# Kernel tuning notes

Hardware: AMD Instinct MI355X
Metric: run time of the kernel (lower is better)

The kernel has to match this reference:

```python
import jax, jax.numpy as jnp
import numpy as np

B, S, D, H = 4, 2048, 1024, 16
DK = D // H

def setup_inputs() -> dict:
    key = jax.random.key(0)
    ks = jax.random.split(key, 8)
    scale = 1.0 / np.sqrt(D)
    return {
        "q": jax.random.normal(ks[0], (B, S, D), jnp.float32),
        "k": jax.random.normal(ks[1], (B, S, D), jnp.float32),
        "v": jax.random.normal(ks[2], (B, S, D), jnp.float32),
        "wq": jax.random.normal(ks[3], (D, D), jnp.float32) * scale,
        "bq": jnp.zeros((D,), jnp.float32),
        "wk": jax.random.normal(ks[4], (D, D), jnp.float32) * scale,
        "bk": jnp.zeros((D,), jnp.float32),
        "wv": jax.random.normal(ks[5], (D, D), jnp.float32) * scale,
        "bv": jnp.zeros((D,), jnp.float32),
        "wo": jax.random.normal(ks[6], (D, D), jnp.float32) * scale,
        "bo": jnp.zeros((D,), jnp.float32),
    }

def reference(q, k, v, wq, bq, wk, bk, wv, bv, wo, bo):
    b, s, _ = q.shape
    # projections; split heads -> [b, h, s, d_k]
    def proj(x, w, bias):
        y = x @ w + bias
        return y.reshape(b, -1, H, DK).transpose(0, 2, 1, 3)
    qh, kh, vh = proj(q, wq, bq), proj(k, wk, bk), proj(v, wv, bv)
    scores = jnp.einsum("bhqd,bhkd->bhqk", qh, kh) / np.sqrt(DK).astype(jnp.float32)
    attn = jax.nn.softmax(scores, axis=-1)  # dropout = identity (eval mode)
    out = jnp.einsum("bhqk,bhkd->bhqd", attn, vh)
    out = out.transpose(0, 2, 1, 3).reshape(b, s, D)
    return out @ wo + bo
```

## Files before the change

kernel.cpp:

```cpp
#include <hip/hip_runtime.h>
#include <hip/hip_bf16.h>

#define B_   4
#define S_   2048
#define D_   1024
#define H_   16
#define DK_  64
#define NTOK 8192

typedef __bf16 bf16_t;
typedef __bf16 bf16x8 __attribute__((ext_vector_type(8)));
typedef __bf16 bf16x4 __attribute__((ext_vector_type(4)));
typedef short  s16x4  __attribute__((ext_vector_type(4)));
typedef float  f32x4  __attribute__((ext_vector_type(4)));

__device__ __forceinline__ void gll16(const void* g, void* l) {
  __builtin_amdgcn_global_load_lds(
      (const __attribute__((address_space(1))) void*)g,
      (__attribute__((address_space(3))) void*)l,
      16, 0, 0);
}

__device__ __forceinline__ f32x4 mfma32(bf16x8 a, bf16x8 b, f32x4 c) {
  return __builtin_amdgcn_mfma_f32_16x16x32_bf16(a, b, c, 0, 0, 0);
}

__device__ __forceinline__ f32x4 mfma16k(bf16x4 a, bf16x4 b, f32x4 c) {
#if defined(__HIP_DEVICE_COMPILE__)
  return __builtin_amdgcn_mfma_f32_16x16x16bf16_1k(
      __builtin_bit_cast(s16x4, a), __builtin_bit_cast(s16x4, b), c, 0, 0, 0);
#else
  (void)a; (void)b;
  return c;
#endif
}

__device__ __forceinline__ float fast_exp2(float x) {
#if defined(__HIP_DEVICE_COMPILE__) && __has_builtin(__builtin_amdgcn_exp2f)
  return __builtin_amdgcn_exp2f(x);
#else
  return exp2f(x);
#endif
}

__global__ __launch_bounds__(256) void tobf16(
    const float* __restrict__ q, const float* __restrict__ k,
    const float* __restrict__ v, bf16_t* __restrict__ o) {
  const float* src = (blockIdx.z == 0) ? q : (blockIdx.z == 1) ? k : v;
  bf16_t* dst = o + (size_t)blockIdx.z * 8388608;
  size_t i = ((size_t)blockIdx.x * 256 + threadIdx.x) * 4;
  float4 x = *(const float4*)&src[i];
  bf16x4 y;
  y[0] = (bf16_t)x.x; y[1] = (bf16_t)x.y;
  y[2] = (bf16_t)x.z; y[3] = (bf16_t)x.w;
  *(bf16x4*)&dst[i] = y;
}

__global__ __launch_bounds__(256) void prep_weights(
    const float* __restrict__ wq, const float* __restrict__ wk,
    const float* __restrict__ wv, const float* __restrict__ wo,
    bf16_t* __restrict__ wtHi) {
  const int z = blockIdx.z;
  const float* W = (z == 0) ? wq : (z == 1) ? wk : (z == 2) ? wv : wo;
  const int k0 = blockIdx.x * 64;
  const int n0 = blockIdx.y * 64;
  const int t = threadIdx.x;
  __shared__ float T[64][65];
#pragma unroll
  for (int rr = 0; rr < 4; ++rr) {
    int row = rr * 16 + (t >> 4);
    int cc = (t & 15) * 4;
    const float4 v = *(const float4*)&W[(size_t)(k0 + row) * D_ + n0 + cc];
    T[row][cc + 0] = v.x; T[row][cc + 1] = v.y;
    T[row][cc + 2] = v.z; T[row][cc + 3] = v.w;
  }
  __syncthreads();
  const int n = t >> 2;
  const int kc = (t & 3) * 16;
  bf16x8 h0, h1;
#pragma unroll
  for (int j = 0; j < 16; ++j) {
    float vv = T[kc + j][n];
    if (j < 8) h0[j] = (bf16_t)vv;
    else       h1[j - 8] = (bf16_t)vv;
  }
  size_t ofs = (size_t)z * 1048576 + (size_t)(n0 + n) * D_ + k0 + kc;
  *(bf16x8*)&wtHi[ofs] = h0; *(bf16x8*)&wtHi[ofs + 8] = h1;
}

__global__ __launch_bounds__(256) void gemm_qkv_bf16(
    const bf16_t* __restrict__ Abf,
    const float* __restrict__ bq, const float* __restrict__ bk,
    const float* __restrict__ bv,
    const bf16_t* __restrict__ wtHi, bf16_t* __restrict__ outQKV) {
  const int z = blockIdx.z;
  const bf16_t* A   = Abf + (size_t)z * 8388608;
  const float* bias = (z == 0) ? bq : (z == 1) ? bk : bv;
  const bf16_t* WHi = wtHi + (size_t)z * 1048576;
  bf16_t* Out = outQKV + (size_t)z * 8388608;

  const int row0 = blockIdx.x * 128;
  const int col0 = blockIdx.y * 128;
  const int t = threadIdx.x;
  const int w = t >> 6, L = t & 63;
  const int m = L & 15, g = L >> 4;

  __shared__ __align__(16) bf16_t As2[128 * 32];
  __shared__ __align__(16) bf16_t Whi_s[128 * 32];

  f32x4 acc[4][4];
#pragma unroll
  for (int i = 0; i < 4; ++i)
#pragma unroll
    for (int j = 0; j < 4; ++j) acc[i][j] = (f32x4){0.f, 0.f, 0.f, 0.f};

  const int aw0 = (w & 1) * 64;
  const int bw0 = (w >> 1) * 64;

  for (int kt = 0; kt < 32; ++kt) {
    const int k0 = kt * 32;
#pragma unroll
    for (int rr = 0; rr < 2; ++rr) {
      int lin16 = rr * 256 + t;
      int n = lin16 >> 2;
      int c = (lin16 & 3) ^ ((n >> 1) & 3);
      gll16(&A[(size_t)(row0 + n) * D_ + k0 + c * 8], &As2[rr * 2048 + w * 512]);
      gll16(&WHi[(size_t)(col0 + n) * D_ + k0 + c * 8], &Whi_s[rr * 2048 + w * 512]);
    }
    __syncthreads();

    bf16x8 af[4], wh[4];
#pragma unroll
    for (int it = 0; it < 4; ++it) {
      int row = aw0 + it * 16 + m;
      int sl = (g ^ ((m >> 1) & 3)) * 8;
      af[it] = *(const bf16x8*)&As2[row * 32 + sl];
    }
#pragma unroll
    for (int jt = 0; jt < 4; ++jt) {
      int n = bw0 + jt * 16 + m;
      int sl = (g ^ ((m >> 1) & 3)) * 8;
      wh[jt] = *(const bf16x8*)&Whi_s[n * 32 + sl];
    }
#pragma unroll
    for (int it = 0; it < 4; ++it)
#pragma unroll
      for (int jt = 0; jt < 4; ++jt)
        acc[it][jt] = mfma32(af[it], wh[jt], acc[it][jt]);
    __syncthreads();
  }
#pragma unroll
  for (int jt = 0; jt < 4; ++jt) {
    int col = col0 + bw0 + jt * 16 + m;
    float bcol = bias[col];
    int h = col >> 6, d = col & 63;
#pragma unroll
    for (int it = 0; it < 4; ++it) {
      if (z != 2) {
#pragma unroll
        for (int r = 0; r < 4; ++r) {
          int row = row0 + aw0 + it * 16 + g * 4 + r;
          int b = row >> 11, s = row & 2047;
          Out[((size_t)((b * H_ + h) * S_ + s)) * DK_ + d] =
              (bf16_t)(acc[it][jt][r] + bcol);
        }
      } else {
        int row = row0 + aw0 + it * 16 + g * 4;
        int b = row >> 11, s = row & 2047;
        bf16x4 p4;
#pragma unroll
        for (int r = 0; r < 4; ++r) p4[r] = (bf16_t)(acc[it][jt][r] + bcol);
        *(bf16x4*)&Out[((size_t)((b * H_ + h) * DK_ + d)) * S_ + s] = p4;
      }
    }
  }
}

__global__ __launch_bounds__(256) void gemm_qkv_f32(
    const float* __restrict__ Aq, const float* __restrict__ Ak,
    const float* __restrict__ Av,
    const float* __restrict__ bq, const float* __restrict__ bk,
    const float* __restrict__ bv,
    const bf16_t* __restrict__ wtHi, bf16_t* __restrict__ outQKV) {
  const int z = blockIdx.z;
  const float* A    = (z == 0) ? Aq : (z == 1) ? Ak : Av;
  const float* bias = (z == 0) ? bq : (z == 1) ? bk : bv;
  const bf16_t* WHi = wtHi + (size_t)z * 1048576;
  bf16_t* Out = outQKV + (size_t)z * 8388608;

  const int row0 = blockIdx.x * 128;
  const int col0 = blockIdx.y * 128;
  const int t = threadIdx.x;
  const int w = t >> 6, L = t & 63;
  const int m = L & 15, g = L >> 4;

  __shared__ __align__(16) float  As[128 * 32];
  __shared__ __align__(16) bf16_t Whi_s[128 * 32];

  f32x4 acc[4][4];
#pragma unroll
  for (int i = 0; i < 4; ++i)
#pragma unroll
    for (int j = 0; j < 4; ++j) acc[i][j] = (f32x4){0.f, 0.f, 0.f, 0.f};

  const int aw0 = (w & 1) * 64;
  const int bw0 = (w >> 1) * 64;

  for (int kt = 0; kt < 32; ++kt) {
    const int k0 = kt * 32;
#pragma unroll
    for (int rr = 0; rr < 4; ++rr) {
      int lin16 = rr * 256 + t;
      int row = lin16 >> 3;
      int c = (lin16 & 7) ^ (row & 7);
      gll16(&A[(size_t)(row0 + row) * D_ + k0 + c * 4], &As[rr * 1024 + w * 256]);
    }
#pragma unroll
    for (int rr = 0; rr < 2; ++rr) {
      int lin16 = rr * 256 + t;
      int n = lin16 >> 2;
      int c = (lin16 & 3) ^ ((n >> 1) & 3);
      gll16(&WHi[(size_t)(col0 + n) * D_ + k0 + c * 8], &Whi_s[rr * 2048 + w * 512]);
    }
    __syncthreads();

    bf16x8 af[4], wh[4];
#pragma unroll
    for (int it = 0; it < 4; ++it) {
      int row = aw0 + it * 16 + m;
      const f32x4* p = (const f32x4*)&As[row * 32];
      f32x4 x0 = p[(2 * g) ^ (m & 7)];
      f32x4 x1 = p[(2 * g + 1) ^ (m & 7)];
      bf16x8 a;
      a[0] = (bf16_t)x0.x; a[1] = (bf16_t)x0.y; a[2] = (bf16_t)x0.z; a[3] = (bf16_t)x0.w;
      a[4] = (bf16_t)x1.x; a[5] = (bf16_t)x1.y; a[6] = (bf16_t)x1.z; a[7] = (bf16_t)x1.w;
      af[it] = a;
    }
#pragma unroll
    for (int jt = 0; jt < 4; ++jt) {
      int n = bw0 + jt * 16 + m;
      int sl = (g ^ ((m >> 1) & 3)) * 8;
      wh[jt] = *(const bf16x8*)&Whi_s[n * 32 + sl];
    }
#pragma unroll
    for (int it = 0; it < 4; ++it)
#pragma unroll
      for (int jt = 0; jt < 4; ++jt)
        acc[it][jt] = mfma32(af[it], wh[jt], acc[it][jt]);
    __syncthreads();
  }
#pragma unroll
  for (int jt = 0; jt < 4; ++jt) {
    int col = col0 + bw0 + jt * 16 + m;
    float bcol = bias[col];
    int h = col >> 6, d = col & 63;
#pragma unroll
    for (int it = 0; it < 4; ++it) {
      if (z != 2) {
#pragma unroll
        for (int r = 0; r < 4; ++r) {
          int row = row0 + aw0 + it * 16 + g * 4 + r;
          int b = row >> 11, s = row & 2047;
          Out[((size_t)((b * H_ + h) * S_ + s)) * DK_ + d] =
              (bf16_t)(acc[it][jt][r] + bcol);
        }
      } else {
        int row = row0 + aw0 + it * 16 + g * 4;
        int b = row >> 11, s = row & 2047;
        bf16x4 p4;
#pragma unroll
        for (int r = 0; r < 4; ++r) p4[r] = (bf16_t)(acc[it][jt][r] + bcol);
        *(bf16x4*)&Out[((size_t)((b * H_ + h) * DK_ + d)) * S_ + s] = p4;
      }
    }
  }
}

__global__ __launch_bounds__(256) void attn(
    const bf16_t* __restrict__ Qh, const bf16_t* __restrict__ Kh,
    const bf16_t* __restrict__ VhT, bf16_t* __restrict__ Ohi) {
  const int bh = blockIdx.y;
  const int q0 = blockIdx.x * 128;
  const int t = threadIdx.x, w = t >> 6, L = t & 63;
  const int m = L & 15, g = L >> 4;

  __shared__ __align__(16) bf16_t Ks[64 * 64];
  __shared__ __align__(16) bf16_t Vt[64 * 64];

  const size_t qbase = (size_t)bh * S_ * DK_;
  const size_t vbase = (size_t)bh * DK_ * S_;

  bf16x8 qf[2][2];
#pragma unroll
  for (int qt = 0; qt < 2; ++qt)
#pragma unroll
    for (int kc = 0; kc < 2; ++kc) {
      int srow = q0 + w * 32 + qt * 16 + m;
      bf16x8 v = *(const bf16x8*)&Qh[qbase + (size_t)srow * DK_ + kc * 32 + g * 8];
#pragma unroll
      for (int j = 0; j < 8; ++j) v[j] = (bf16_t)(0.18033688f * (float)v[j]);
      qf[qt][kc] = v;
    }

  const bf16x4 ones = {(bf16_t)1.f, (bf16_t)1.f, (bf16_t)1.f, (bf16_t)1.f};

  f32x4 oacc[2][4];
  f32x4 lacc[2];
#pragma unroll
  for (int qt = 0; qt < 2; ++qt) {
#pragma unroll
    for (int dt = 0; dt < 4; ++dt) oacc[qt][dt] = (f32x4){0.f, 0.f, 0.f, 0.f};
    lacc[qt] = (f32x4){0.f, 0.f, 0.f, 0.f};
  }

  for (int kv0 = 0; kv0 < S_; kv0 += 64) {
#pragma unroll
    for (int rr = 0; rr < 2; ++rr) {
      int lin16 = rr * 256 + t;
      int rrow = lin16 >> 3;
      int c = (lin16 & 7) ^ (rrow & 7);
      gll16(&Kh[qbase + (size_t)(kv0 + rrow) * DK_ + c * 8], &Ks[rr * 2048 + w * 512]);
      gll16(&VhT[vbase + (size_t)rrow * S_ + kv0 + c * 8], &Vt[rr * 2048 + w * 512]);
    }
    __syncthreads();

    f32x4 sc[2][4];
#pragma unroll
    for (int kvt = 0; kvt < 4; ++kvt) {
      int n = kvt * 16 + m;
      bf16x8 kf0 = *(const bf16x8*)&Ks[n * 64 + ((g) ^ (n & 7)) * 8];
      bf16x8 kf1 = *(const bf16x8*)&Ks[n * 64 + ((4 + g) ^ (n & 7)) * 8];
#pragma unroll
      for (int qt = 0; qt < 2; ++qt) {
        f32x4 z4 = (f32x4){0.f, 0.f, 0.f, 0.f};
        z4 = mfma32(kf0, qf[qt][0], z4);
        z4 = mfma32(kf1, qf[qt][1], z4);
        sc[qt][kvt] = z4;
      }
    }

    bf16x4 pb[2][4];
#pragma unroll
    for (int qt = 0; qt < 2; ++qt)
#pragma unroll
      for (int kvt = 0; kvt < 4; ++kvt) {
        bf16x4 p4;
#pragma unroll
        for (int r = 0; r < 4; ++r) p4[r] = (bf16_t)fast_exp2(sc[qt][kvt][r]);
        pb[qt][kvt] = p4;
      }

#pragma unroll
    for (int kvt = 0; kvt < 4; ++kvt) {
#pragma unroll
      for (int qt = 0; qt < 2; ++qt)
        lacc[qt] = mfma16k(ones, pb[qt][kvt], lacc[qt]);
#pragma unroll
      for (int dt = 0; dt < 4; ++dt) {
        int d = dt * 16 + m;
        int sl = (kvt * 2 + (g >> 1)) ^ (d & 7);
        bf16x4 vf = *(const bf16x4*)&Vt[d * 64 + sl * 8 + (g & 1) * 4];
#pragma unroll
        for (int qt = 0; qt < 2; ++qt)
          oacc[qt][dt] = mfma16k(vf, pb[qt][kvt], oacc[qt][dt]);
      }
    }
    __syncthreads();
  }

  const int b = bh >> 4, h = bh & 15;
#pragma unroll
  for (int qt = 0; qt < 2; ++qt) {
    float inv = 1.f / lacc[qt][0];
    int srow = q0 + w * 32 + qt * 16 + m;
    size_t rowofs = ((size_t)(b * S_ + srow)) * D_ + h * DK_;
#pragma unroll
    for (int dt = 0; dt < 4; ++dt) {
      bf16x4 hp;
#pragma unroll
      for (int r = 0; r < 4; ++r) hp[r] = (bf16_t)(oacc[qt][dt][r] * inv);
      *(bf16x4*)&Ohi[rowofs + dt * 16 + g * 4] = hp;
    }
  }
}

__global__ __launch_bounds__(256) void gemm_out(
    const bf16_t* __restrict__ Ahi, const bf16_t* __restrict__ wtHi,
    const float* __restrict__ bias, float* __restrict__ Out) {
  const bf16_t* WHi = wtHi + (size_t)3 * 1048576;
  const int row0 = blockIdx.x * 128;
  const int col0 = blockIdx.y * 128;
  const int t = threadIdx.x;
  const int w = t >> 6, L = t & 63;
  const int m = L & 15, g = L >> 4;

  __shared__ __align__(16) bf16_t Ahi_s[128 * 32];
  __shared__ __align__(16) bf16_t Whi_s[128 * 32];

  f32x4 acc[4][4];
#pragma unroll
  for (int i = 0; i < 4; ++i)
#pragma unroll
    for (int j = 0; j < 4; ++j) acc[i][j] = (f32x4){0.f, 0.f, 0.f, 0.f};

  const int aw0 = (w & 1) * 64;
  const int bw0 = (w >> 1) * 64;

  for (int kt = 0; kt < 32; ++kt) {
    const int k0 = kt * 32;
#pragma unroll
    for (int rr = 0; rr < 2; ++rr) {
      int lin16 = rr * 256 + t;
      int n = lin16 >> 2;
      int c = (lin16 & 3) ^ ((n >> 1) & 3);
      gll16(&Ahi[(size_t)(row0 + n) * D_ + k0 + c * 8], &Ahi_s[rr * 2048 + w * 512]);
      gll16(&WHi[(size_t)(col0 + n) * D_ + k0 + c * 8], &Whi_s[rr * 2048 + w * 512]);
    }
    __syncthreads();

    bf16x8 ah[4], wh[4];
#pragma unroll
    for (int it = 0; it < 4; ++it) {
      int row = aw0 + it * 16 + m;
      int sl = (g ^ ((m >> 1) & 3)) * 8;
      ah[it] = *(const bf16x8*)&Ahi_s[row * 32 + sl];
    }
#pragma unroll
    for (int jt = 0; jt < 4; ++jt) {
      int n = bw0 + jt * 16 + m;
      int sl = (g ^ ((m >> 1) & 3)) * 8;
      wh[jt] = *(const bf16x8*)&Whi_s[n * 32 + sl];
    }
#pragma unroll
    for (int it = 0; it < 4; ++it)
#pragma unroll
      for (int jt = 0; jt < 4; ++jt)
        acc[it][jt] = mfma32(ah[it], wh[jt], acc[it][jt]);
    __syncthreads();
  }
#pragma unroll
  for (int jt = 0; jt < 4; ++jt) {
    int col = col0 + bw0 + jt * 16 + m;
    float bcol = bias[col];
#pragma unroll
    for (int it = 0; it < 4; ++it)
#pragma unroll
      for (int r = 0; r < 4; ++r) {
        int row = row0 + aw0 + it * 16 + g * 4 + r;
        Out[(size_t)row * D_ + col] = acc[it][jt][r] + bcol;
      }
  }
}

extern "C" void kernel_launch(void* const* d_in, const int* in_sizes, int n_in,
                              void* d_out, int out_size, void* d_ws, size_t ws_size,
                              hipStream_t stream) {
  const float* q  = (const float*)d_in[0];
  const float* k  = (const float*)d_in[1];
  const float* v  = (const float*)d_in[2];
  const float* wq = (const float*)d_in[3];
  const float* bq = (const float*)d_in[4];
  const float* wk = (const float*)d_in[5];
  const float* bk = (const float*)d_in[6];
  const float* wv = (const float*)d_in[7];
  const float* bv = (const float*)d_in[8];
  const float* wo = (const float*)d_in[9];
  const float* bo = (const float*)d_in[10];
  float* out = (float*)d_out;

  char* ws = (char*)d_ws;
  bf16_t* wtHi = (bf16_t*)(ws);
  bf16_t* QKVh = (bf16_t*)(ws + (8ull << 20));
  bf16_t* Ohi  = (bf16_t*)(ws + (56ull << 20));
  bf16_t* Abf  = (bf16_t*)(ws + (56ull << 20));

  const bool big = ws_size >= (104ull << 20);

  hipLaunchKernelGGL(prep_weights, dim3(16, 16, 4), dim3(256), 0, stream,
                     wq, wk, wv, wo, wtHi);
  if (big) {
    hipLaunchKernelGGL(tobf16, dim3(8192, 1, 3), dim3(256), 0, stream,
                       q, k, v, Abf);
    hipLaunchKernelGGL(gemm_qkv_bf16, dim3(64, 8, 3), dim3(256), 0, stream,
                       Abf, bq, bk, bv, wtHi, QKVh);
  } else {
    hipLaunchKernelGGL(gemm_qkv_f32, dim3(64, 8, 3), dim3(256), 0, stream,
                       q, k, v, bq, bk, bv, wtHi, QKVh);
  }
  hipLaunchKernelGGL(attn, dim3(16, 64), dim3(256), 0, stream,
                     QKVh, QKVh + 8388608, QKVh + 16777216, Ohi);
  hipLaunchKernelGGL(gemm_out, dim3(64, 8), dim3(256), 0, stream,
                     Ohi, wtHi, bo, out);
}
```

Baseline: 373.3 us.

## Switch attention kernel to 32x32x16 MFMA with permlane32 swap for P operand

Rewrites the attention inner loop to use 32x32x16 bf16 MFMA tiles instead of 16x16x32 for QK^T and 16x16x16 for PV. Scores are exponentiated, packed to bf16 and rearranged across lane halves with permlane32_swap so the score accumulator layout can be fed straight back as the B operand of the PV and row-sum MFMAs. Launch bounds now request two blocks per CU. The aim is fewer MFMA issues and fewer LDS reads per tile, at the cost of larger 16-wide accumulators and higher register pressure.

```diff
diff --git a/kernel.cpp b/kernel.cpp
--- a/kernel.cpp
+++ b/kernel.cpp
@@ -11,8 +11,11 @@
 typedef __bf16 bf16_t;
 typedef __bf16 bf16x8 __attribute__((ext_vector_type(8)));
 typedef __bf16 bf16x4 __attribute__((ext_vector_type(4)));
-typedef short  s16x4  __attribute__((ext_vector_type(4)));
+typedef __bf16 bf16x2 __attribute__((ext_vector_type(2)));
 typedef float  f32x4  __attribute__((ext_vector_type(4)));
+typedef float  f32x16 __attribute__((ext_vector_type(16)));
+typedef unsigned u32x4 __attribute__((ext_vector_type(4)));
+typedef int    i32x2  __attribute__((ext_vector_type(2)));
 
 __device__ __forceinline__ void gll16(const void* g, void* l) {
   __builtin_amdgcn_global_load_lds(
@@ -25,10 +28,9 @@
   return __builtin_amdgcn_mfma_f32_16x16x32_bf16(a, b, c, 0, 0, 0);
 }
 
-__device__ __forceinline__ f32x4 mfma16k(bf16x4 a, bf16x4 b, f32x4 c) {
+__device__ __forceinline__ f32x16 mfma32x32(bf16x8 a, bf16x8 b, f32x16 c) {
 #if defined(__HIP_DEVICE_COMPILE__)
-  return __builtin_amdgcn_mfma_f32_16x16x16bf16_1k(
-      __builtin_bit_cast(s16x4, a), __builtin_bit_cast(s16x4, b), c, 0, 0, 0);
+  return __builtin_amdgcn_mfma_f32_32x32x16_bf16(a, b, c, 0, 0, 0);
 #else
   (void)a; (void)b;
   return c;
@@ -41,6 +43,47 @@
 #else
   return exp2f(x);
 #endif
+}
+
+__device__ __forceinline__ f32x16 zero16() {
+  f32x16 z;
+#pragma unroll
+  for (int i = 0; i < 16; ++i) z[i] = 0.f;
+  return z;
+}
+
+__device__ __forceinline__ unsigned pkbf(float lo, float hi) {
+  bf16x2 t;
+  t[0] = (bf16_t)lo;
+  t[1] = (bf16_t)hi;
+  return __builtin_bit_cast(unsigned, t);
+}
+
+__device__ __forceinline__ void plswap(unsigned &x, unsigned &y) {
+#if defined(__HIP_DEVICE_COMPILE__)
+  i32x2 r = __builtin_amdgcn_permlane32_swap((int)x, (int)y, false, false);
+  x = (unsigned)r[0];
+  y = (unsigned)r[1];
+#endif
+}
+
+__device__ __forceinline__ void build_pa(const f32x16 s, bf16x8 &p0, bf16x8 &p1) {
+  unsigned A0 = pkbf(fast_exp2(s[0]),  fast_exp2(s[1]));
+  unsigned A1 = pkbf(fast_exp2(s[2]),  fast_exp2(s[3]));
+  unsigned B0 = pkbf(fast_exp2(s[4]),  fast_exp2(s[5]));
+  unsigned B1 = pkbf(fast_exp2(s[6]),  fast_exp2(s[7]));
+  unsigned C0 = pkbf(fast_exp2(s[8]),  fast_exp2(s[9]));
+  unsigned C1 = pkbf(fast_exp2(s[10]), fast_exp2(s[11]));
+  unsigned D0 = pkbf(fast_exp2(s[12]), fast_exp2(s[13]));
+  unsigned D1 = pkbf(fast_exp2(s[14]), fast_exp2(s[15]));
+  plswap(A0, B0);
+  plswap(A1, B1);
+  plswap(C0, D0);
+  plswap(C1, D1);
+  u32x4 lo = {A0, A1, B0, B1};
+  u32x4 hi = {C0, C1, D0, D1};
+  p0 = __builtin_bit_cast(bf16x8, lo);
+  p1 = __builtin_bit_cast(bf16x8, hi);
 }
 
 __global__ __launch_bounds__(256) void tobf16(
@@ -276,13 +319,14 @@
   }
 }
 
-__global__ __launch_bounds__(256) void attn(
+__global__ __launch_bounds__(256, 2) void attn(
     const bf16_t* __restrict__ Qh, const bf16_t* __restrict__ Kh,
     const bf16_t* __restrict__ VhT, bf16_t* __restrict__ Ohi) {
   const int bh = blockIdx.y;
   const int q0 = blockIdx.x * 128;
-  const int t = threadIdx.x, w = t >> 6, L = t & 63;
-  const int m = L & 15, g = L >> 4;
+  const int t = threadIdx.x, w = t >> 6;
+  const int lane = t & 63;
+  const int lo5 = lane & 31, hi = lane >> 5;
 
   __shared__ __align__(16) bf16_t Ks[64 * 64];
   __shared__ __align__(16) bf16_t Vt[64 * 64];
@@ -290,28 +334,26 @@
   const size_t qbase = (size_t)bh * S_ * DK_;
   const size_t vbase = (size_t)bh * DK_ * S_;
 
-  bf16x8 qf[2][2];
-#pragma unroll
-  for (int qt = 0; qt < 2; ++qt)
-#pragma unroll
-    for (int kc = 0; kc < 2; ++kc) {
-      int srow = q0 + w * 32 + qt * 16 + m;
-      bf16x8 v = *(const bf16x8*)&Qh[qbase + (size_t)srow * DK_ + kc * 32 + g * 8];
-#pragma unroll
-      for (int j = 0; j < 8; ++j) v[j] = (bf16_t)(0.18033688f * (float)v[j]);
-      qf[qt][kc] = v;
-    }
-
-  const bf16x4 ones = {(bf16_t)1.f, (bf16_t)1.f, (bf16_t)1.f, (bf16_t)1.f};
-
-  f32x4 oacc[2][4];
-  f32x4 lacc[2];
-#pragma unroll
-  for (int qt = 0; qt < 2; ++qt) {
-#pragma unroll
-    for (int dt = 0; dt < 4; ++dt) oacc[qt][dt] = (f32x4){0.f, 0.f, 0.f, 0.f};
-    lacc[qt] = (f32x4){0.f, 0.f, 0.f, 0.f};
-  }
+  const int qrow = q0 + w * 32 + lo5;
+  bf16x8 qf[4];
+#pragma unroll
+  for (int ks = 0; ks < 4; ++ks) {
+    bf16x8 v = *(const bf16x8*)&Qh[qbase + (size_t)qrow * DK_ + ks * 16 + hi * 8];
+#pragma unroll
+    for (int j = 0; j < 8; ++j) v[j] = (bf16_t)(0.18033688f * (float)v[j]);
+    qf[ks] = v;
+  }
+
+  bf16x8 ones;
+#pragma unroll
+  for (int j = 0; j < 8; ++j) ones[j] = (bf16_t)1.f;
+
+  int offs[4];
+#pragma unroll
+  for (int ks = 0; ks < 4; ++ks)
+    offs[ks] = lo5 * 64 + (((ks * 2 + hi) ^ (lo5 & 7)) * 8);
+
+  f32x16 oacc0 = zero16(), oacc1 = zero16(), lacc = zero16();
 
   for (int kv0 = 0; kv0 < S_; kv0 += 64) {
 #pragma unroll
@@ -324,63 +366,44 @@
     }
     __syncthreads();
 
-    f32x4 sc[2][4];
-#pragma unroll
-    for (int kvt = 0; kvt < 4; ++kvt) {
-      int n = kvt * 16 + m;
-      bf16x8 kf0 = *(const bf16x8*)&Ks[n * 64 + ((g) ^ (n & 7)) * 8];
-      bf16x8 kf1 = *(const bf16x8*)&Ks[n * 64 + ((4 + g) ^ (n & 7)) * 8];
-#pragma unroll
-      for (int qt = 0; qt < 2; ++qt) {
-        f32x4 z4 = (f32x4){0.f, 0.f, 0.f, 0.f};
-        z4 = mfma32(kf0, qf[qt][0], z4);
-        z4 = mfma32(kf1, qf[qt][1], z4);
-        sc[qt][kvt] = z4;
-      }
-    }
-
-    bf16x4 pb[2][4];
-#pragma unroll
-    for (int qt = 0; qt < 2; ++qt)
-#pragma unroll
-      for (int kvt = 0; kvt < 4; ++kvt) {
-        bf16x4 p4;
-#pragma unroll
-        for (int r = 0; r < 4; ++r) p4[r] = (bf16_t)fast_exp2(sc[qt][kvt][r]);
-        pb[qt][kvt] = p4;
-      }
-
-#pragma unroll
-    for (int kvt = 0; kvt < 4; ++kvt) {
-#pragma unroll
-      for (int qt = 0; qt < 2; ++qt)
-        lacc[qt] = mfma16k(ones, pb[qt][kvt], lacc[qt]);
-#pragma unroll
-      for (int dt = 0; dt < 4; ++dt) {
-        int d = dt * 16 + m;
-        int sl = (kvt * 2 + (g >> 1)) ^ (d & 7);
-        bf16x4 vf = *(const bf16x4*)&Vt[d * 64 + sl * 8 + (g & 1) * 4];
-#pragma unroll
-        for (int qt = 0; qt < 2; ++qt)
-          oacc[qt][dt] = mfma16k(vf, pb[qt][kvt], oacc[qt][dt]);
-      }
+    f32x16 sc0 = zero16(), sc1 = zero16();
+#pragma unroll
+    for (int ks = 0; ks < 4; ++ks) {
+      bf16x8 k0 = *(const bf16x8*)&Ks[offs[ks]];
+      bf16x8 k1 = *(const bf16x8*)&Ks[offs[ks] + 2048];
+      sc0 = mfma32x32(k0, qf[ks], sc0);
+      sc1 = mfma32x32(k1, qf[ks], sc1);
+    }
+
+    bf16x8 pa0, pa1, pa2, pa3;
+    build_pa(sc0, pa0, pa1);
+    build_pa(sc1, pa2, pa3);
+
+#pragma unroll
+    for (int ks = 0; ks < 4; ++ks) {
+      bf16x8 pb = (ks == 0) ? pa0 : (ks == 1) ? pa1 : (ks == 2) ? pa2 : pa3;
+      lacc = mfma32x32(ones, pb, lacc);
+      bf16x8 v0 = *(const bf16x8*)&Vt[offs[ks]];
+      bf16x8 v1 = *(const bf16x8*)&Vt[offs[ks] + 2048];
+      oacc0 = mfma32x32(v0, pb, oacc0);
+      oacc1 = mfma32x32(v1, pb, oacc1);
     }
     __syncthreads();
   }
 
   const int b = bh >> 4, h = bh & 15;
-#pragma unroll
-  for (int qt = 0; qt < 2; ++qt) {
-    float inv = 1.f / lacc[qt][0];
-    int srow = q0 + w * 32 + qt * 16 + m;
-    size_t rowofs = ((size_t)(b * S_ + srow)) * D_ + h * DK_;
-#pragma unroll
-    for (int dt = 0; dt < 4; ++dt) {
-      bf16x4 hp;
-#pragma unroll
-      for (int r = 0; r < 4; ++r) hp[r] = (bf16_t)(oacc[qt][dt][r] * inv);
-      *(bf16x4*)&Ohi[rowofs + dt * 16 + g * 4] = hp;
-    }
+  const float inv = 1.f / lacc[0];
+  const size_t rowofs = ((size_t)(b * S_ + qrow)) * D_ + h * DK_;
+#pragma unroll
+  for (int rg = 0; rg < 4; ++rg) {
+    bf16x4 o0, o1;
+#pragma unroll
+    for (int j = 0; j < 4; ++j) {
+      o0[j] = (bf16_t)(oacc0[rg * 4 + j] * inv);
+      o1[j] = (bf16_t)(oacc1[rg * 4 + j] * inv);
+    }
+    *(bf16x4*)&Ohi[rowofs + rg * 8 + hi * 4] = o0;
+    *(bf16x4*)&Ohi[rowofs + 32 + rg * 8 + hi * 4] = o1;
   }
 }
 
```

Result: faster. 350.2 us (-6.2%).
